# Optimization experiments

Measured on AMD Instinct MI355X. Metric: run time of the kernel, lower is better.

## Reference

```python
import jax, jax.numpy as jnp
import numpy as np

EMBED_DIM = 1024
NUM_HEADS = 16
HEAD_DIM = EMBED_DIM // NUM_HEADS
B, T = 2, 2048


def setup_inputs() -> dict:
    key = jax.random.key(0)
    kx, kqkv, kout = jax.random.split(key, 3)
    x = jax.random.normal(kx, (B, T, EMBED_DIM), dtype=jnp.float32)
    # torch Linear(in, out, bias=False): y = x @ W.T, W ~ U(-1/sqrt(in), 1/sqrt(in)).
    # Store pre-transposed as (in, out) for direct matmul.
    bound = 1.0 / np.sqrt(EMBED_DIM)
    w_qkv = jax.random.uniform(kqkv, (EMBED_DIM, 3 * EMBED_DIM), dtype=jnp.float32, minval=-bound, maxval=bound)
    w_out = jax.random.uniform(kout, (EMBED_DIM, EMBED_DIM), dtype=jnp.float32, minval=-bound, maxval=bound)
    return {"x": x, "w_qkv": w_qkv, "w_out": w_out}


def reference(x, w_qkv, w_out):
    Bx, Tx, C = x.shape
    qkv = x @ w_qkv  # (B, T, 3C)
    q, k, v = jnp.split(qkv, 3, axis=-1)

    def split_heads(t):
        return t.reshape(Bx, Tx, NUM_HEADS, HEAD_DIM).transpose(0, 2, 1, 3)  # (B,H,T,hd)

    q, k, v = split_heads(q), split_heads(k), split_heads(v)
    scale = 1.0 / jnp.sqrt(jnp.float32(HEAD_DIM))
    scores = jnp.einsum("bhqd,bhkd->bhqk", q, k) * scale  # (B,H,T,T)
    causal = jnp.tril(jnp.ones((Tx, Tx), dtype=bool))  # True = keep
    scores = jnp.where(causal, scores, jnp.float32(-jnp.inf))
    weights = jax.nn.softmax(scores, axis=-1)
    out = jnp.einsum("bhqk,bhkd->bhqd", weights, v)  # (B,H,T,hd)
    out = out.transpose(0, 2, 1, 3).reshape(Bx, Tx, C)
    return out @ w_out
```

## Files before the change

### kernel.cpp

```cpp
#include <hip/hip_runtime.h>
#include <hip/hip_bf16.h>
#include <stdint.h>
#include <math.h>

#define B_ 2
#define T_ 2048
#define C_ 1024
#define H_ 16
#define HD_ 64
#define BT_ (B_*T_)
#define N1_ (3*C_)

typedef unsigned short u16;
typedef uint32_t u32;
typedef __attribute__((ext_vector_type(8))) short bf16x8;
typedef __attribute__((ext_vector_type(4))) float f32x4;
typedef __attribute__((ext_vector_type(16))) float f32x16;
typedef __attribute__((ext_vector_type(4))) unsigned int u32x4;

__device__ __forceinline__ u16 f2bf(float f) {
  __hip_bfloat16 h = __float2bfloat16(f);
  return *reinterpret_cast<u16*>(&h);
}
__device__ __forceinline__ float bf2f(u16 u) {
  u32 w = ((u32)u) << 16;
  return *reinterpret_cast<float*>(&w);
}
__device__ __forceinline__ u32 cvtpk(float lo, float hi) {
  u32 r;
  asm("v_cvt_pk_bf16_f32 %0, %1, %2" : "=v"(r) : "v"(lo), "v"(hi));
  return r;
}
__device__ __forceinline__ float exp2v(float x) {
  float r;
  asm("v_exp_f32 %0, %1" : "=v"(r) : "v"(x));
  return r;
}

__device__ __forceinline__ void gload_lds16(const void* g, void* l) {
  __builtin_amdgcn_global_load_lds(
      (const __attribute__((address_space(1))) uint32_t*)g,
      (__attribute__((address_space(3))) uint32_t*)l, 16, 0, 0);
}

#define BARX() do { asm volatile("" ::: "memory"); __builtin_amdgcn_s_barrier(); \
                    asm volatile("" ::: "memory"); } while (0)
#define LGKM0() do { asm volatile("s_waitcnt lgkmcnt(0)" ::: "memory"); \
                     __builtin_amdgcn_sched_barrier(0); } while (0)

__global__ __launch_bounds__(256) void prep_k(const float* __restrict__ x,
                                              const float* __restrict__ w_qkv,
                                              const float* __restrict__ w_out,
                                              u16* __restrict__ xb,
                                              u16* __restrict__ wqkvT,
                                              u16* __restrict__ woutT) {
  __shared__ float tile[32][33];
  int bid = blockIdx.x;
  if (bid < 4096) {
    int idx = bid * 1024 + threadIdx.x * 4;
    float4 v = *reinterpret_cast<const float4*>(x + idx);
    u16 tmp[4] = {f2bf(v.x), f2bf(v.y), f2bf(v.z), f2bf(v.w)};
    *reinterpret_cast<uint2*>(xb + idx) = *reinterpret_cast<const uint2*>(tmp);
    return;
  }
  const float* w;
  u16* wt;
  int N, tb;
  if (bid < 7168) { tb = bid - 4096; w = w_qkv; wt = wqkvT; N = N1_; }
  else            { tb = bid - 7168; w = w_out; wt = woutT; N = C_;  }
  int nx = N >> 5;
  int n0 = (tb % nx) * 32, k0 = (tb / nx) * 32;
  int tx = threadIdx.x & 31, ty = threadIdx.x >> 5;
#pragma unroll
  for (int i = 0; i < 4; i++)
    tile[ty + i*8][tx] = w[(size_t)(k0 + ty + i*8) * N + n0 + tx];
  __syncthreads();
#pragma unroll
  for (int i = 0; i < 4; i++)
    wt[(size_t)(n0 + ty + i*8) * 1024 + k0 + tx] = f2bf(tile[tx][ty + i*8]);
}

__global__ __launch_bounds__(512, 2) void gemm256(const u16* __restrict__ A, const u16* __restrict__ Bt,
                                                  u16* __restrict__ Cc) {
  __shared__ u16 As[2][256*64];
  __shared__ u16 Bs[2][192*64];
  int tid = threadIdx.x, w = tid >> 6, lane = tid & 63;
  int m0 = blockIdx.y * 256, n0 = blockIdx.x * 192;
  int wm = (w >> 2) * 128, wn = (w & 3) * 48;
  f32x4 acc[8][3] = {};

  size_t aoff[4];
  size_t boff[3];
#pragma unroll
  for (int i = 0; i < 4; i++) {
    int c = i*512 + tid, row = c >> 3;
    aoff[i] = (size_t)(m0 + row) * 1024 + (size_t)((((c & 7) ^ (row & 7))) * 8);
  }
#pragma unroll
  for (int i = 0; i < 3; i++) {
    int c = i*512 + tid, row = c >> 3;
    boff[i] = (size_t)(n0 + row) * 1024 + (size_t)((((c & 7) ^ (row & 7))) * 8);
  }
  int dstc = w * 1024;

  int r15 = lane & 15, kq = lane >> 4;
  int slot0 = (kq ^ (r15 & 7)) * 8;
  int abase = (wm + r15) * 64;
  int bbase = (wn + r15) * 64;

#pragma unroll
  for (int i = 0; i < 4; i++)
    gload_lds16(A + aoff[i], (char*)&As[0][0] + i*8192 + dstc);
#pragma unroll
  for (int i = 0; i < 3; i++)
    gload_lds16(Bt + boff[i], (char*)&Bs[0][0] + i*8192 + dstc);

  for (int t = 0; t < 16; ++t) {
    int buf = t & 1;
    const u16* Ab = &As[buf][0];
    const u16* Bb = &Bs[buf][0];
    int slot1 = slot0 ^ 32;
    bf16x8 af[8], bfv[3];

    asm volatile("s_waitcnt vmcnt(0)" ::: "memory");
    BARX();

#pragma unroll
    for (int nf = 0; nf < 3; nf++) bfv[nf] = *reinterpret_cast<const bf16x8*>(&Bb[bbase + nf*1024 + slot0]);
#pragma unroll
    for (int mf = 0; mf < 8; mf++) af[mf] = *reinterpret_cast<const bf16x8*>(&Ab[abase + mf*1024 + slot0]);
    if (t < 15) {
      int ko = (t + 1) * 64;
#pragma unroll
      for (int i = 0; i < 4; i++)
        gload_lds16(A + aoff[i] + ko, (char*)&As[buf ^ 1][0] + i*8192 + dstc);
#pragma unroll
      for (int i = 0; i < 3; i++)
        gload_lds16(Bt + boff[i] + ko, (char*)&Bs[buf ^ 1][0] + i*8192 + dstc);
    }
    BARX();
    LGKM0();
    __builtin_amdgcn_s_setprio(1);
#pragma unroll
    for (int mf = 0; mf < 8; mf++)
#pragma unroll
      for (int nf = 0; nf < 3; nf++)
        acc[mf][nf] = __builtin_amdgcn_mfma_f32_16x16x32_bf16(af[mf], bfv[nf], acc[mf][nf], 0, 0, 0);
    __builtin_amdgcn_s_setprio(0);

#pragma unroll
    for (int nf = 0; nf < 3; nf++) bfv[nf] = *reinterpret_cast<const bf16x8*>(&Bb[bbase + nf*1024 + slot1]);
#pragma unroll
    for (int mf = 0; mf < 8; mf++) af[mf] = *reinterpret_cast<const bf16x8*>(&Ab[abase + mf*1024 + slot1]);
    BARX();
    LGKM0();
    __builtin_amdgcn_s_setprio(1);
#pragma unroll
    for (int mf = 0; mf < 8; mf++)
#pragma unroll
      for (int nf = 0; nf < 3; nf++)
        acc[mf][nf] = __builtin_amdgcn_mfma_f32_16x16x32_bf16(af[mf], bfv[nf], acc[mf][nf], 0, 0, 0);
    __builtin_amdgcn_s_setprio(0);
  }

  int rg = kq * 4;
#pragma unroll
  for (int mf = 0; mf < 8; mf++)
#pragma unroll
    for (int nf = 0; nf < 3; nf++) {
      size_t basei = (size_t)(m0 + wm + mf*16 + rg) * N1_ + (size_t)(n0 + wn + nf*16 + r15);
#pragma unroll
      for (int r = 0; r < 4; r++)
        Cc[basei + (size_t)r * N1_] = f2bf(acc[mf][nf][r]);
    }
}

template<int OUTF32>
__global__ __launch_bounds__(256) void gemm_bt(const u16* __restrict__ A, const u16* __restrict__ Bt,
                                               void* __restrict__ Cv, int M, int N, int K) {
  __shared__ u16 As[2][128*32];
  __shared__ u16 Bs[2][128*32];
  int tid = threadIdx.x, wave = tid >> 6, lane = tid & 63;
  int m0 = blockIdx.y * 128, n0 = blockIdx.x * 128;
  int wm = (wave >> 1) * 64, wn = (wave & 1) * 64;
  f32x4 acc[4][4] = {};
  int srow = lane >> 2, scol = (lane & 3) * 8;
  int fro  = (lane & 15) * 32 + (lane >> 4) * 8;

  auto stage = [&](int k0, int buf) {
#pragma unroll
    for (int i = 0; i < 2; i++) {
      gload_lds16(A  + (size_t)(m0 + i*64 + wave*16 + srow) * K + k0 + scol, &As[buf][(i*64 + wave*16) * 32]);
      gload_lds16(Bt + (size_t)(n0 + i*64 + wave*16 + srow) * K + k0 + scol, &Bs[buf][(i*64 + wave*16) * 32]);
    }
  };

  stage(0, 0);
  int nk = K >> 5;
  for (int it = 0; it < nk; ++it) {
    int cur = it & 1;
    asm volatile("s_waitcnt vmcnt(0)" ::: "memory");
    BARX();
    bf16x8 af[4], bfr[4];
#pragma unroll
    for (int i = 0; i < 4; i++) af[i]  = *reinterpret_cast<const bf16x8*>(&As[cur][(wm + i*16)*32 + fro]);
#pragma unroll
    for (int j2 = 0; j2 < 4; j2++) bfr[j2] = *reinterpret_cast<const bf16x8*>(&Bs[cur][(wn + j2*16)*32 + fro]);
    if (it + 1 < nk) stage((it + 1) << 5, cur ^ 1);
    BARX();
    LGKM0();
    __builtin_amdgcn_s_setprio(1);
#pragma unroll
    for (int i = 0; i < 4; i++)
#pragma unroll
      for (int j2 = 0; j2 < 4; j2++)
        acc[i][j2] = __builtin_amdgcn_mfma_f32_16x16x32_bf16(af[i], bfr[j2], acc[i][j2], 0, 0, 0);
    __builtin_amdgcn_s_setprio(0);
  }
  int rg = (lane >> 4) * 4, cq = lane & 15;
#pragma unroll
  for (int i = 0; i < 4; i++)
#pragma unroll
    for (int j2 = 0; j2 < 4; j2++) {
      size_t basei = (size_t)(m0 + wm + i*16 + rg) * N + (size_t)(n0 + wn + j2*16 + cq);
#pragma unroll
      for (int r = 0; r < 4; r++) {
        if constexpr (OUTF32) ((float*)Cv)[basei + (size_t)r * N] = acc[i][j2][r];
        else                  ((u16*)Cv)[basei + (size_t)r * N]   = f2bf(acc[i][j2][r]);
      }
    }
}

__global__ __launch_bounds__(192, 3) void attn_kernel(const u16* __restrict__ qkv, u16* __restrict__ attnout) {
  __shared__ u16 Sm[3][4096];
  int tid = threadIdx.x;
  int w = tid >> 6, lane = tid & 63;
  int q31 = lane & 31, hi = lane >> 5;
  int lid = blockIdx.x;
  int xcd = lid & 7, j = lid >> 3;
  int bh = xcd * 4 + (j & 3);
  int p = j >> 2;
  int b = bh >> 4, h = bh & 15;
  const u16* base = qkv + (size_t)b * T_ * N1_;

  u16* Ks = Sm[w];
  u32* Vt32 = reinterpret_cast<u32*>(Sm[w] + 2048);

  const u16* ksrc = base + C_ + h*HD_ + (size_t)(lane >> 3) * N1_
                    + (size_t)(((lane & 7) ^ ((lane >> 3) & 7)) * 8);
  int kp2 = lane & 15, dc = (lane >> 4) * 16;
  int vcs = kp2 >> 2, vkl = kp2 & 3;
  int vflip = (lane >> 4) & 1;
  const u16* vsrc = base + 2*C_ + h*HD_ + (size_t)(2*kp2) * N1_ + dc;
  const float QSC = 0.125f * 1.44269504088896f;
  int swr = (q31 >> 1) & 3;
  int q31f = q31 ^ ((q31 >> 4) & 1);

  for (int sp = 0; sp < 2; sp++) {
    int strip = sp ? p : (63 - p);
    int qbase = strip * 32;
    int qg = qbase + q31;
    int nkt = strip + 1;

    f32x16 oacc[2] = {};
    float l_run = 0.f;

    if (w < nkt) {
      bf16x8 qf[4];
      {
        const u16* qrow = base + (size_t)qg * N1_ + h * HD_;
#pragma unroll
        for (int kk = 0; kk < 4; kk++) {
          bf16x8 raw = *reinterpret_cast<const bf16x8*>(qrow + kk*16 + hi*8);
          const u16* rp = (const u16*)&raw;
          u32x4 qp;
#pragma unroll
          for (int jj = 0; jj < 4; jj++)
            qp[jj] = cvtpk(bf2f(rp[2*jj]) * QSC, bf2f(rp[2*jj+1]) * QSC);
          qf[kk] = __builtin_bit_cast(bf16x8, qp);
        }
      }

      bf16x8 vA[2], vB[2];
      {
        size_t off0 = (size_t)(w * 32) * N1_;
#pragma unroll
        for (int r = 0; r < 4; r++)
          gload_lds16(ksrc + off0 + (size_t)(8*r) * N1_, (char*)Ks + r*1024);
#pragma unroll
        for (int r = 0; r < 2; r++) {
          vA[r] = *reinterpret_cast<const bf16x8*>(vsrc + off0 + r*8);
          vB[r] = *reinterpret_cast<const bf16x8*>(vsrc + off0 + r*8 + N1_);
        }
      }

      for (int kt = w; kt < nkt; kt += 3) {
        int kb = kt * 32;
        bool lastown  = (kt + 3 >= nkt);
        bool masktile = (kt == nkt - 1);

        asm volatile("s_waitcnt vmcnt(0)" ::: "memory");

#pragma unroll
        for (int r2 = 0; r2 < 2; r2++) {
          const u16* au = (const u16*)&vA[r2];
          const u16* bu = (const u16*)&vB[r2];
#pragma unroll
          for (int i = 0; i < 8; i++) {
            int d = dc + r2*8 + i;
            Vt32[(d ^ vflip)*16 + ((vcs ^ ((d>>1)&3)) << 2) + vkl] = (u32)au[i] | ((u32)bu[i] << 16);
          }
        }

        f32x16 st = {};
#pragma unroll
        for (int kk = 0; kk < 4; kk++) {
          bf16x8 kf = *reinterpret_cast<const bf16x8*>(
              &Ks[q31*64 + ((((kk<<1) | hi) ^ (q31 & 7)) << 3)]);
          st = __builtin_amdgcn_mfma_f32_32x32x16_bf16(kf, qf[kk], st, 0, 0, 0);
        }
        asm volatile("s_waitcnt lgkmcnt(0)" ::: "memory");
        __builtin_amdgcn_sched_barrier(0);

        if (!lastown) {
          size_t off = (size_t)(kb + 96) * N1_;
#pragma unroll
          for (int r = 0; r < 4; r++)
            gload_lds16(ksrc + off + (size_t)(8*r) * N1_, (char*)Ks + r*1024);
#pragma unroll
          for (int r = 0; r < 2; r++) {
            vA[r] = *reinterpret_cast<const bf16x8*>(vsrc + off + r*8);
            vB[r] = *reinterpret_cast<const bf16x8*>(vsrc + off + r*8 + N1_);
          }
        }

        if (masktile) {
#pragma unroll
          for (int r = 0; r < 16; r++) {
            int keyg = kb + (r&3) + 8*(r>>2) + 4*hi;
            if (keyg > qg) st[r] = -__builtin_inff();
          }
        }
        float tsum = 0.f;
#pragma unroll
        for (int r = 0; r < 16; r++) {
          float pp = exp2v(st[r]);
          st[r] = pp;
          tsum += pp;
        }
        l_run += tsum;

        u32 pk[8];
#pragma unroll
        for (int m = 0; m < 8; m++) pk[m] = cvtpk(st[2*m], st[2*m+1]);
        asm volatile("v_permlane32_swap_b32 %0, %1" : "+v"(pk[0]), "+v"(pk[2]));
        asm volatile("v_permlane32_swap_b32 %0, %1" : "+v"(pk[1]), "+v"(pk[3]));
        asm volatile("v_permlane32_swap_b32 %0, %1" : "+v"(pk[4]), "+v"(pk[6]));
        asm volatile("v_permlane32_swap_b32 %0, %1" : "+v"(pk[5]), "+v"(pk[7]));
        u32x4 fr0 = { pk[0], pk[1], pk[2], pk[3] };
        u32x4 fr1 = { pk[4], pk[5], pk[6], pk[7] };
        bf16x8 pf0 = __builtin_bit_cast(bf16x8, fr0);
        bf16x8 pf1 = __builtin_bit_cast(bf16x8, fr1);

#pragma unroll
        for (int dt = 0; dt < 2; dt++)
#pragma unroll
          for (int kc = 0; kc < 2; kc++) {
            int cs = (kc << 1) | hi;
            bf16x8 vf = *reinterpret_cast<const bf16x8*>(
                &Vt32[(32*dt + q31f)*16 + ((cs ^ swr) << 2)]);
            oacc[dt] = __builtin_amdgcn_mfma_f32_32x32x16_bf16(vf, kc ? pf1 : pf0, oacc[dt], 0, 0, 0);
          }
      }
      l_run += __shfl_xor(l_run, 32);
    }

    __syncthreads();
    if (w) {
      float* park = (float*)Sm[w];
#pragma unroll
      for (int dt = 0; dt < 2; dt++)
#pragma unroll
        for (int r = 0; r < 16; r++) park[(dt*16 + r)*64 + lane] = oacc[dt][r];
      float* ml = (float*)Sm[0];
      ml[(w-1)*64 + lane] = l_run;
    }
    __syncthreads();
    if (w == 0) {
      const float* ml = (const float*)Sm[0];
      float linv = 1.f / (l_run + ml[lane] + ml[64 + lane]);
      const float* p1 = (const float*)Sm[1];
      const float* p2 = (const float*)Sm[2];
      u16* orow = attnout + (size_t)(b*T_ + qg) * C_ + h*HD_;
#pragma unroll
      for (int dt = 0; dt < 2; dt++)
#pragma unroll
        for (int m = 0; m < 8; m++) {
          int e0 = (dt*16 + 2*m)*64 + lane, e1 = e0 + 64;
          float v0 = (oacc[dt][2*m]   + p1[e0] + p2[e0]) * linv;
          float v1 = (oacc[dt][2*m+1] + p1[e1] + p2[e1]) * linv;
          int d = 32*dt + 2*(m&1) + 8*(m>>1) + 4*hi;
          *reinterpret_cast<u32*>(orow + d) = cvtpk(v0, v1);
        }
    }
    __syncthreads();
  }
}

extern "C" void kernel_launch(void* const* d_in, const int* in_sizes, int n_in,
                              void* d_out, int out_size, void* d_ws, size_t ws_size,
                              hipStream_t stream) {
  const float* x     = (const float*)d_in[0];
  const float* w_qkv = (const float*)d_in[1];
  const float* w_out = (const float*)d_in[2];
  float* out = (float*)d_out;
  char* ws = (char*)d_ws;
  u16* xb    = (u16*)(ws);
  u16* wqkvT = (u16*)(ws + ((size_t)8  << 20));
  u16* woutT = (u16*)(ws + ((size_t)14 << 20));
  u16* qkvb  = (u16*)(ws + ((size_t)16 << 20));
  u16* attnb = (u16*)(ws + ((size_t)40 << 20));

  prep_k<<<8192, 256, 0, stream>>>(x, w_qkv, w_out, xb, wqkvT, woutT);
  gemm256<<<dim3(16, 16), 512, 0, stream>>>(xb, wqkvT, qkvb);
  attn_kernel<<<1024, 192, 0, stream>>>(qkvb, attnb);
  gemm_bt<1><<<dim3(C_/128, BT_/128), 256, 0, stream>>>(attnb, woutT, (void*)out, BT_, C_, C_);
}
```

Baseline: 113.6 us.

## Fuse paired causal strips into one K/V pass sharing loaded tiles

The attention kernel used to process its two query strips (63-p and p) one after the other, reloading K and V tiles for each. Now both strips run in a single loop over the longer strip's key tiles. Each K/V tile is loaded and transposed into LDS once and feeds MFMAs for both strips while the short strip is still active. This cuts the global and LDS traffic and the loop overhead spent on the shorter strip. The cost is about twice the accumulator and Q-fragment registers, which may lower occupancy or cause spills, plus an extra branch per iteration.

```diff
diff --git a/kernel.cpp b/kernel.cpp
--- a/kernel.cpp
+++ b/kernel.cpp
@@ -256,154 +256,241 @@
   int swr = (q31 >> 1) & 3;
   int q31f = q31 ^ ((q31 >> 4) & 1);
 
-  for (int sp = 0; sp < 2; sp++) {
-    int strip = sp ? p : (63 - p);
-    int qbase = strip * 32;
-    int qg = qbase + q31;
-    int nkt = strip + 1;
-
-    f32x16 oacc[2] = {};
-    float l_run = 0.f;
-
-    if (w < nkt) {
-      bf16x8 qf[4];
+  int sA = 63 - p, sB = p;
+  int qgA = sA * 32 + q31, qgB = sB * 32 + q31;
+  int nktU = sA + 1;
+
+  bf16x8 qfA[4], qfB[4];
+  {
+    const u16* qrowA = base + (size_t)qgA * N1_ + h * HD_;
+    const u16* qrowB = base + (size_t)qgB * N1_ + h * HD_;
+#pragma unroll
+    for (int kk = 0; kk < 4; kk++) {
+      bf16x8 ra = *reinterpret_cast<const bf16x8*>(qrowA + kk*16 + hi*8);
+      bf16x8 rb = *reinterpret_cast<const bf16x8*>(qrowB + kk*16 + hi*8);
+      const u16* pa = (const u16*)&ra;
+      const u16* pb = (const u16*)&rb;
+      u32x4 qa, qb;
+#pragma unroll
+      for (int jj = 0; jj < 4; jj++) {
+        qa[jj] = cvtpk(bf2f(pa[2*jj]) * QSC, bf2f(pa[2*jj+1]) * QSC);
+        qb[jj] = cvtpk(bf2f(pb[2*jj]) * QSC, bf2f(pb[2*jj+1]) * QSC);
+      }
+      qfA[kk] = __builtin_bit_cast(bf16x8, qa);
+      qfB[kk] = __builtin_bit_cast(bf16x8, qb);
+    }
+  }
+
+  f32x16 oaccA[2] = {}, oaccB[2] = {};
+  float lA = 0.f, lB = 0.f;
+
+  bf16x8 vA[2], vB[2];
+  {
+    size_t off0 = (size_t)(w * 32) * N1_;
+#pragma unroll
+    for (int r = 0; r < 4; r++)
+      gload_lds16(ksrc + off0 + (size_t)(8*r) * N1_, (char*)Ks + r*1024);
+#pragma unroll
+    for (int r = 0; r < 2; r++) {
+      vA[r] = *reinterpret_cast<const bf16x8*>(vsrc + off0 + r*8);
+      vB[r] = *reinterpret_cast<const bf16x8*>(vsrc + off0 + r*8 + N1_);
+    }
+  }
+
+  for (int kt = w; kt < nktU; kt += 3) {
+    int kb = kt * 32;
+    bool lastown = (kt + 3 >= nktU);
+    bool actB = (kt <= sB);
+
+    asm volatile("s_waitcnt vmcnt(0)" ::: "memory");
+
+#pragma unroll
+    for (int r2 = 0; r2 < 2; r2++) {
+      const u16* au = (const u16*)&vA[r2];
+      const u16* bu = (const u16*)&vB[r2];
+#pragma unroll
+      for (int i = 0; i < 8; i++) {
+        int d = dc + r2*8 + i;
+        Vt32[(d ^ vflip)*16 + ((vcs ^ ((d>>1)&3)) << 2) + vkl] = (u32)au[i] | ((u32)bu[i] << 16);
+      }
+    }
+
+    f32x16 stA = {}, stB = {};
+    if (actB) {
+#pragma unroll
+      for (int kk = 0; kk < 4; kk++) {
+        bf16x8 kf = *reinterpret_cast<const bf16x8*>(
+            &Ks[q31*64 + ((((kk<<1) | hi) ^ (q31 & 7)) << 3)]);
+        stA = __builtin_amdgcn_mfma_f32_32x32x16_bf16(kf, qfA[kk], stA, 0, 0, 0);
+        stB = __builtin_amdgcn_mfma_f32_32x32x16_bf16(kf, qfB[kk], stB, 0, 0, 0);
+      }
+    } else {
+#pragma unroll
+      for (int kk = 0; kk < 4; kk++) {
+        bf16x8 kf = *reinterpret_cast<const bf16x8*>(
+            &Ks[q31*64 + ((((kk<<1) | hi) ^ (q31 & 7)) << 3)]);
+        stA = __builtin_amdgcn_mfma_f32_32x32x16_bf16(kf, qfA[kk], stA, 0, 0, 0);
+      }
+    }
+    asm volatile("s_waitcnt lgkmcnt(0)" ::: "memory");
+    __builtin_amdgcn_sched_barrier(0);
+
+    if (!lastown) {
+      size_t off = (size_t)(kb + 96) * N1_;
+#pragma unroll
+      for (int r = 0; r < 4; r++)
+        gload_lds16(ksrc + off + (size_t)(8*r) * N1_, (char*)Ks + r*1024);
+#pragma unroll
+      for (int r = 0; r < 2; r++) {
+        vA[r] = *reinterpret_cast<const bf16x8*>(vsrc + off + r*8);
+        vB[r] = *reinterpret_cast<const bf16x8*>(vsrc + off + r*8 + N1_);
+      }
+    }
+
+    if (kt == sA) {
+#pragma unroll
+      for (int r = 0; r < 16; r++) {
+        int keyg = kb + (r&3) + 8*(r>>2) + 4*hi;
+        if (keyg > qgA) stA[r] = -__builtin_inff();
+      }
+    }
+    {
+      float ts = 0.f;
+#pragma unroll
+      for (int r = 0; r < 16; r++) {
+        float pp = exp2v(stA[r]);
+        stA[r] = pp;
+        ts += pp;
+      }
+      lA += ts;
+    }
+    bf16x8 pfA0, pfA1;
+    {
+      u32 pk[8];
+#pragma unroll
+      for (int m = 0; m < 8; m++) pk[m] = cvtpk(stA[2*m], stA[2*m+1]);
+      asm volatile("v_permlane32_swap_b32 %0, %1" : "+v"(pk[0]), "+v"(pk[2]));
+      asm volatile("v_permlane32_swap_b32 %0, %1" : "+v"(pk[1]), "+v"(pk[3]));
+      asm volatile("v_permlane32_swap_b32 %0, %1" : "+v"(pk[4]), "+v"(pk[6]));
+      asm volatile("v_permlane32_swap_b32 %0, %1" : "+v"(pk[5]), "+v"(pk[7]));
+      u32x4 f0 = { pk[0], pk[1], pk[2], pk[3] };
+      u32x4 f1 = { pk[4], pk[5], pk[6], pk[7] };
+      pfA0 = __builtin_bit_cast(bf16x8, f0);
+      pfA1 = __builtin_bit_cast(bf16x8, f1);
+    }
+
+    if (actB) {
+      if (kt == sB) {
+#pragma unroll
+        for (int r = 0; r < 16; r++) {
+          int keyg = kb + (r&3) + 8*(r>>2) + 4*hi;
+          if (keyg > qgB) stB[r] = -__builtin_inff();
+        }
+      }
       {
-        const u16* qrow = base + (size_t)qg * N1_ + h * HD_;
-#pragma unroll
-        for (int kk = 0; kk < 4; kk++) {
-          bf16x8 raw = *reinterpret_cast<const bf16x8*>(qrow + kk*16 + hi*8);
-          const u16* rp = (const u16*)&raw;
-          u32x4 qp;
-#pragma unroll
-          for (int jj = 0; jj < 4; jj++)
-            qp[jj] = cvtpk(bf2f(rp[2*jj]) * QSC, bf2f(rp[2*jj+1]) * QSC);
-          qf[kk] = __builtin_bit_cast(bf16x8, qp);
+        float ts = 0.f;
+#pragma unroll
+        for (int r = 0; r < 16; r++) {
+          float pp = exp2v(stB[r]);
+          stB[r] = pp;
+          ts += pp;
         }
-      }
-
-      bf16x8 vA[2], vB[2];
+        lB += ts;
+      }
+      bf16x8 pfB0, pfB1;
       {
-        size_t off0 = (size_t)(w * 32) * N1_;
-#pragma unroll
-        for (int r = 0; r < 4; r++)
-          gload_lds16(ksrc + off0 + (size_t)(8*r) * N1_, (char*)Ks + r*1024);
-#pragma unroll
-        for (int r = 0; r < 2; r++) {
-          vA[r] = *reinterpret_cast<const bf16x8*>(vsrc + off0 + r*8);
-          vB[r] = *reinterpret_cast<const bf16x8*>(vsrc + off0 + r*8 + N1_);
-        }
-      }
-
-      for (int kt = w; kt < nkt; kt += 3) {
-        int kb = kt * 32;
-        bool lastown  = (kt + 3 >= nkt);
-        bool masktile = (kt == nkt - 1);
-
-        asm volatile("s_waitcnt vmcnt(0)" ::: "memory");
-
-#pragma unroll
-        for (int r2 = 0; r2 < 2; r2++) {
-          const u16* au = (const u16*)&vA[r2];
-          const u16* bu = (const u16*)&vB[r2];
-#pragma unroll
-          for (int i = 0; i < 8; i++) {
-            int d = dc + r2*8 + i;
-            Vt32[(d ^ vflip)*16 + ((vcs ^ ((d>>1)&3)) << 2) + vkl] = (u32)au[i] | ((u32)bu[i] << 16);
-          }
-        }
-
-        f32x16 st = {};
-#pragma unroll
-        for (int kk = 0; kk < 4; kk++) {
-          bf16x8 kf = *reinterpret_cast<const bf16x8*>(
-              &Ks[q31*64 + ((((kk<<1) | hi) ^ (q31 & 7)) << 3)]);
-          st = __builtin_amdgcn_mfma_f32_32x32x16_bf16(kf, qf[kk], st, 0, 0, 0);
-        }
-        asm volatile("s_waitcnt lgkmcnt(0)" ::: "memory");
-        __builtin_amdgcn_sched_barrier(0);
-
-        if (!lastown) {
-          size_t off = (size_t)(kb + 96) * N1_;
-#pragma unroll
-          for (int r = 0; r < 4; r++)
-            gload_lds16(ksrc + off + (size_t)(8*r) * N1_, (char*)Ks + r*1024);
-#pragma unroll
-          for (int r = 0; r < 2; r++) {
-            vA[r] = *reinterpret_cast<const bf16x8*>(vsrc + off + r*8);
-            vB[r] = *reinterpret_cast<const bf16x8*>(vsrc + off + r*8 + N1_);
-          }
-        }
-
-        if (masktile) {
-#pragma unroll
-          for (int r = 0; r < 16; r++) {
-            int keyg = kb + (r&3) + 8*(r>>2) + 4*hi;
-            if (keyg > qg) st[r] = -__builtin_inff();
-          }
-        }
-        float tsum = 0.f;
-#pragma unroll
-        for (int r = 0; r < 16; r++) {
-          float pp = exp2v(st[r]);
-          st[r] = pp;
-          tsum += pp;
-        }
-        l_run += tsum;
-
         u32 pk[8];
 #pragma unroll
-        for (int m = 0; m < 8; m++) pk[m] = cvtpk(st[2*m], st[2*m+1]);
+        for (int m = 0; m < 8; m++) pk[m] = cvtpk(stB[2*m], stB[2*m+1]);
         asm volatile("v_permlane32_swap_b32 %0, %1" : "+v"(pk[0]), "+v"(pk[2]));
         asm volatile("v_permlane32_swap_b32 %0, %1" : "+v"(pk[1]), "+v"(pk[3]));
         asm volatile("v_permlane32_swap_b32 %0, %1" : "+v"(pk[4]), "+v"(pk[6]));
         asm volatile("v_permlane32_swap_b32 %0, %1" : "+v"(pk[5]), "+v"(pk[7]));
-        u32x4 fr0 = { pk[0], pk[1], pk[2], pk[3] };
-        u32x4 fr1 = { pk[4], pk[5], pk[6], pk[7] };
-        bf16x8 pf0 = __builtin_bit_cast(bf16x8, fr0);
-        bf16x8 pf1 = __builtin_bit_cast(bf16x8, fr1);
-
-#pragma unroll
-        for (int dt = 0; dt < 2; dt++)
-#pragma unroll
-          for (int kc = 0; kc < 2; kc++) {
-            int cs = (kc << 1) | hi;
-            bf16x8 vf = *reinterpret_cast<const bf16x8*>(
-                &Vt32[(32*dt + q31f)*16 + ((cs ^ swr) << 2)]);
-            oacc[dt] = __builtin_amdgcn_mfma_f32_32x32x16_bf16(vf, kc ? pf1 : pf0, oacc[dt], 0, 0, 0);
-          }
-      }
-      l_run += __shfl_xor(l_run, 32);
-    }
-
-    __syncthreads();
-    if (w) {
-      float* park = (float*)Sm[w];
+        u32x4 f0 = { pk[0], pk[1], pk[2], pk[3] };
+        u32x4 f1 = { pk[4], pk[5], pk[6], pk[7] };
+        pfB0 = __builtin_bit_cast(bf16x8, f0);
+        pfB1 = __builtin_bit_cast(bf16x8, f1);
+      }
 #pragma unroll
       for (int dt = 0; dt < 2; dt++)
 #pragma unroll
-        for (int r = 0; r < 16; r++) park[(dt*16 + r)*64 + lane] = oacc[dt][r];
-      float* ml = (float*)Sm[0];
-      ml[(w-1)*64 + lane] = l_run;
-    }
-    __syncthreads();
-    if (w == 0) {
-      const float* ml = (const float*)Sm[0];
-      float linv = 1.f / (l_run + ml[lane] + ml[64 + lane]);
-      const float* p1 = (const float*)Sm[1];
-      const float* p2 = (const float*)Sm[2];
-      u16* orow = attnout + (size_t)(b*T_ + qg) * C_ + h*HD_;
+        for (int kc = 0; kc < 2; kc++) {
+          int cs = (kc << 1) | hi;
+          bf16x8 vf = *reinterpret_cast<const bf16x8*>(
+              &Vt32[(32*dt + q31f)*16 + ((cs ^ swr) << 2)]);
+          oaccA[dt] = __builtin_amdgcn_mfma_f32_32x32x16_bf16(vf, kc ? pfA1 : pfA0, oaccA[dt], 0, 0, 0);
+          oaccB[dt] = __builtin_amdgcn_mfma_f32_32x32x16_bf16(vf, kc ? pfB1 : pfB0, oaccB[dt], 0, 0, 0);
+        }
+    } else {
 #pragma unroll
       for (int dt = 0; dt < 2; dt++)
 #pragma unroll
-        for (int m = 0; m < 8; m++) {
-          int e0 = (dt*16 + 2*m)*64 + lane, e1 = e0 + 64;
-          float v0 = (oacc[dt][2*m]   + p1[e0] + p2[e0]) * linv;
-          float v1 = (oacc[dt][2*m+1] + p1[e1] + p2[e1]) * linv;
-          int d = 32*dt + 2*(m&1) + 8*(m>>1) + 4*hi;
-          *reinterpret_cast<u32*>(orow + d) = cvtpk(v0, v1);
+        for (int kc = 0; kc < 2; kc++) {
+          int cs = (kc << 1) | hi;
+          bf16x8 vf = *reinterpret_cast<const bf16x8*>(
+              &Vt32[(32*dt + q31f)*16 + ((cs ^ swr) << 2)]);
+          oaccA[dt] = __builtin_amdgcn_mfma_f32_32x32x16_bf16(vf, kc ? pfA1 : pfA0, oaccA[dt], 0, 0, 0);
         }
     }
-    __syncthreads();
+  }
+  lA += __shfl_xor(lA, 32);
+  lB += __shfl_xor(lB, 32);
+
+  __syncthreads();
+  if (w) {
+    float* park = (float*)Sm[w];
+#pragma unroll
+    for (int dt = 0; dt < 2; dt++)
+#pragma unroll
+      for (int r = 0; r < 16; r++) park[(dt*16 + r)*64 + lane] = oaccA[dt][r];
+    float* ml = (float*)Sm[0];
+    ml[(w-1)*64 + lane] = lA;
+  }
+  __syncthreads();
+  if (w == 0) {
+    const float* ml = (const float*)Sm[0];
+    float linv = 1.f / (lA + ml[lane] + ml[64 + lane]);
+    const float* p1 = (const float*)Sm[1];
+    const float* p2 = (const float*)Sm[2];
+    u16* orow = attnout + (size_t)(b*T_ + qgA) * C_ + h*HD_;
+#pragma unroll
+    for (int dt = 0; dt < 2; dt++)
+#pragma unroll
+      for (int m = 0; m < 8; m++) {
+        int e0 = (dt*16 + 2*m)*64 + lane, e1 = e0 + 64;
+        float v0 = (oaccA[dt][2*m]   + p1[e0] + p2[e0]) * linv;
+        float v1 = (oaccA[dt][2*m+1] + p1[e1] + p2[e1]) * linv;
+        int d = 32*dt + 2*(m&1) + 8*(m>>1) + 4*hi;
+        *reinterpret_cast<u32*>(orow + d) = cvtpk(v0, v1);
+      }
+  }
+  __syncthreads();
+  if (w) {
+    float* park = (float*)Sm[w];
+#pragma unroll
+    for (int dt = 0; dt < 2; dt++)
+#pragma unroll
+      for (int r = 0; r < 16; r++) park[(dt*16 + r)*64 + lane] = oaccB[dt][r];
+    float* ml = (float*)Sm[0];
+    ml[(w-1)*64 + lane] = lB;
+  }
+  __syncthreads();
+  if (w == 0) {
+    const float* ml = (const float*)Sm[0];
+    float linv = 1.f / (lB + ml[lane] + ml[64 + lane]);
+    const float* p1 = (const float*)Sm[1];
+    const float* p2 = (const float*)Sm[2];
+    u16* orow = attnout + (size_t)(b*T_ + qgB) * C_ + h*HD_;
+#pragma unroll
+    for (int dt = 0; dt < 2; dt++)
+#pragma unroll
+      for (int m = 0; m < 8; m++) {
+        int e0 = (dt*16 + 2*m)*64 + lane, e1 = e0 + 64;
+        float v0 = (oaccB[dt][2*m]   + p1[e0] + p2[e0]) * linv;
+        float v1 = (oaccB[dt][2*m+1] + p1[e1] + p2[e1]) * linv;
+        int d = 32*dt + 2*(m&1) + 8*(m>>1) + 4*hi;
+        *reinterpret_cast<u32*>(orow + d) = cvtpk(v0, v1);
+      }
   }
 }
 
```

Measured after the change: 112.3 us. About the same (-1.1%).
